# Performance work log

Measured on AMD Instinct MI355X. Metric: run time of the kernel, lower is better.

Reference implementation:

```python
import jax, jax.numpy as jnp
import numpy as np

DIM = 512
HEADS = 8
HEAD_DIM = DIM // HEADS
SCALE = HEAD_DIM ** -0.5
CPB_HIDDEN = 512
N_CLASSES = 2
LN_EPS = 1e-5


def _layernorm(x, g, b):
    m = jnp.mean(x, axis=-1, keepdims=True)
    v = jnp.var(x, axis=-1, keepdims=True)
    return (x - m) / jnp.sqrt(v + LN_EPS) * g + b


def _coord_attention(x, coords, cpb_w1, cpb_b1, cpb_w2, cpb_b2, qkv_w, qkv_b, proj_w, proj_b):
    B, N, C = x.shape
    qkv = (x @ qkv_w + qkv_b).reshape(B, N, 3, HEADS, HEAD_DIM)
    q, k, v = jnp.moveaxis(qkv, 2, 0)  # each (B, N, H, hd)
    attn = jnp.einsum('bnhd,bmhd->bhnm', q * SCALE, k)  # (B, H, N, N)
    rel = coords[:, :, None, :] - coords[:, None, :, :]  # (B, N, N, 2)
    rel = rel / (jnp.linalg.norm(rel, axis=-1, keepdims=True) + 1e-6)
    bias = jax.nn.relu(rel @ cpb_w1 + cpb_b1) @ cpb_w2 + cpb_b2  # (B, N, N, H)
    attn = jax.nn.softmax(attn + jnp.transpose(bias, (0, 3, 1, 2)), axis=-1)
    out = jnp.einsum('bhnm,bmhd->bnhd', attn, v).reshape(B, N, C)
    return out @ proj_w + proj_b


def setup_inputs() -> dict:
    key = jax.random.key(0)
    ks = iter(jax.random.split(key, 32))
    d = {}
    d['h'] = jax.random.normal(next(ks), (1, 400, 1024), dtype=jnp.float32)
    d['coords'] = jax.random.uniform(next(ks), (1, 400, 2), dtype=jnp.float32) * 1000.0
    def lin(kw, kb, fan_in, fan_out):
        w = jax.random.normal(kw, (fan_in, fan_out), dtype=jnp.float32) / np.sqrt(fan_in)
        b = jax.random.normal(kb, (fan_out,), dtype=jnp.float32) * 0.01
        return w, b
    d['fc1_w'], d['fc1_b'] = lin(next(ks), next(ks), 1024, DIM)
    d['cls_token'] = jax.random.normal(next(ks), (1, 1, DIM), dtype=jnp.float32)
    for p in ('l1', 'l2'):
        d[p + '_norm_g'] = jnp.ones((DIM,), jnp.float32)
        d[p + '_norm_b'] = jnp.zeros((DIM,), jnp.float32)
        d[p + '_cpb_w1'], d[p + '_cpb_b1'] = lin(next(ks), next(ks), 2, CPB_HIDDEN)
        d[p + '_cpb_w2'], d[p + '_cpb_b2'] = lin(next(ks), next(ks), CPB_HIDDEN, HEADS)
        d[p + '_qkv_w'], d[p + '_qkv_b'] = lin(next(ks), next(ks), DIM, 3 * DIM)
        d[p + '_proj_w'], d[p + '_proj_b'] = lin(next(ks), next(ks), DIM, DIM)
    d['norm_g'] = jnp.ones((DIM,), jnp.float32)
    d['norm_b'] = jnp.zeros((DIM,), jnp.float32)
    d['fc2_w'], d['fc2_b'] = lin(next(ks), next(ks), DIM, N_CLASSES)
    return d


def reference(h, coords, fc1_w, fc1_b, cls_token,
              l1_norm_g, l1_norm_b, l1_cpb_w1, l1_cpb_b1, l1_cpb_w2, l1_cpb_b2,
              l1_qkv_w, l1_qkv_b, l1_proj_w, l1_proj_b,
              l2_norm_g, l2_norm_b, l2_cpb_w1, l2_cpb_b1, l2_cpb_w2, l2_cpb_b2,
              l2_qkv_w, l2_qkv_b, l2_proj_w, l2_proj_b,
              norm_g, norm_b, fc2_w, fc2_b):
    B, Np, _ = h.shape
    h = jax.nn.relu(h @ fc1_w + fc1_b)  # (B, N, 512)
    side = int(np.ceil(np.sqrt(Np)))
    add = side * side - Np  # pad bag to a perfect square (wrap-around copy)
    h = jnp.concatenate([h, h[:, :add, :]], axis=1)
    coords = jnp.concatenate([coords, coords[:, :add, :]], axis=1)
    cls = jnp.broadcast_to(cls_token, (B, 1, DIM))
    h = jnp.concatenate([cls, h], axis=1)
    coords = jnp.concatenate([jnp.zeros((B, 1, 2), h.dtype), coords], axis=1)
    h = h + _coord_attention(_layernorm(h, l1_norm_g, l1_norm_b), coords,
                             l1_cpb_w1, l1_cpb_b1, l1_cpb_w2, l1_cpb_b2,
                             l1_qkv_w, l1_qkv_b, l1_proj_w, l1_proj_b)
    h = h + _coord_attention(_layernorm(h, l2_norm_g, l2_norm_b), coords,
                             l2_cpb_w1, l2_cpb_b1, l2_cpb_w2, l2_cpb_b2,
                             l2_qkv_w, l2_qkv_b, l2_proj_w, l2_proj_b)
    h = _layernorm(h, norm_g, norm_b)[:, 0]  # CLS token
    return h @ fc2_w + fc2_b  # (B, n_classes)
```

## Files before the change

### kernel.cpp

```cpp
#include <hip/hip_runtime.h>
#include <math.h>

#define NP 401
#define DIM 512
#define HEADS 8
#define HD 64
#define LN_EPS 1e-5f
#define ATT_SCALE 0.125f
#define SP 448
#define PLANE (NP * SP)
#define CPB_M 16384
#define TSTRIDE (CPB_M + 64)
#define PS (401L * 1536)

template<bool TB, typename LA, typename LB>
__device__ __forceinline__ void gemm64(
    int kBeg, int kEnd, int tid,
    float (*as)[68], float (*bs)[68], float (&acc)[4][4],
    LA&& loadA, LB&& loadB)
{
    float aR[4], bR[4];
    loadA(kBeg, aR);
    loadB(kBeg, bR);
    for (int k0 = kBeg; k0 < kEnd; k0 += 16) {
        const int arow = tid >> 2, aq = tid & 3;
        as[aq * 4 + 0][arow] = aR[0];
        as[aq * 4 + 1][arow] = aR[1];
        as[aq * 4 + 2][arow] = aR[2];
        as[aq * 4 + 3][arow] = aR[3];
        if (!TB) {
            *(float4*)&bs[tid >> 4][(tid & 15) * 4] =
                make_float4(bR[0], bR[1], bR[2], bR[3]);
        } else {
            bs[aq * 4 + 0][arow] = bR[0];
            bs[aq * 4 + 1][arow] = bR[1];
            bs[aq * 4 + 2][arow] = bR[2];
            bs[aq * 4 + 3][arow] = bR[3];
        }
        __syncthreads();
        float nA[4] = {0.f,0.f,0.f,0.f}, nB[4] = {0.f,0.f,0.f,0.f};
        if (k0 + 16 < kEnd) { loadA(k0 + 16, nA); loadB(k0 + 16, nB); }
        const int tx = tid & 15, ty = tid >> 4;
        #pragma unroll
        for (int kk = 0; kk < 16; ++kk) {
            float4 a4 = *(const float4*)&as[kk][ty * 4];
            float4 b4 = *(const float4*)&bs[kk][tx * 4];
            float av[4] = {a4.x, a4.y, a4.z, a4.w};
            float bv[4] = {b4.x, b4.y, b4.z, b4.w};
            #pragma unroll
            for (int r = 0; r < 4; ++r)
                #pragma unroll
                for (int c = 0; c < 4; ++c)
                    acc[r][c] = fmaf(av[r], bv[c], acc[r][c]);
        }
        __syncthreads();
        #pragma unroll
        for (int j = 0; j < 4; ++j) { aR[j] = nA[j]; bR[j] = nB[j]; }
    }
}

__global__ __launch_bounds__(256) void gemm_split_kernel(
    const float* __restrict__ A, int lda,
    const float* __restrict__ B, int ldb,
    float* __restrict__ P, int ldc, long slice,
    int M, int N, int K, int skN)
{
    __shared__ float as[16][68], bs[16][68];
    const int tid = threadIdx.x;
    const int m0 = blockIdx.x * 64, n0 = blockIdx.y * 64;
    const int sk = blockIdx.z;
    const int KS = ((K + skN * 16 - 1) / (skN * 16)) * 16;
    const int kBeg = sk * KS;
    const int kEnd = (kBeg + KS < K) ? kBeg + KS : K;
    float acc[4][4] = {};

    auto loadA = [&](int k0, float r[4]) {
        r[0] = r[1] = r[2] = r[3] = 0.f;
        int gm = m0 + (tid >> 2);
        if (gm >= M) return;
        int gk = k0 + (tid & 3) * 4;
        const float* p = A + (long)gm * lda + gk;
        if (gk + 3 < kEnd) {
            float4 v = *(const float4*)p;
            r[0] = v.x; r[1] = v.y; r[2] = v.z; r[3] = v.w;
        } else {
            #pragma unroll
            for (int j = 0; j < 4; ++j) if (gk + j < kEnd) r[j] = p[j];
        }
    };
    auto loadB = [&](int k0, float r[4]) {
        r[0] = r[1] = r[2] = r[3] = 0.f;
        int gk = k0 + (tid >> 4);
        if (gk >= kEnd) return;
        int gn = n0 + (tid & 15) * 4;
        const float* p = B + (long)gk * ldb + gn;
        if (gn + 3 < N) {
            float4 v = *(const float4*)p;
            r[0] = v.x; r[1] = v.y; r[2] = v.z; r[3] = v.w;
        } else {
            #pragma unroll
            for (int j = 0; j < 4; ++j) if (gn + j < N) r[j] = p[j];
        }
    };
    if (kBeg < kEnd)
        gemm64<false>(kBeg, kEnd, tid, as, bs, acc, loadA, loadB);

    float* C = P + (long)sk * slice;
    const int tx = tid & 15, ty = tid >> 4;
    #pragma unroll
    for (int r = 0; r < 4; ++r) {
        int m = m0 + ty * 4 + r;
        if (m >= M) continue;
        int n = n0 + tx * 4;
        if (n + 3 < N) {
            *(float4*)&C[(long)m * ldc + n] =
                make_float4(acc[r][0], acc[r][1], acc[r][2], acc[r][3]);
        } else {
            #pragma unroll
            for (int c = 0; c < 4; ++c)
                if (n + c < N) C[(long)m * ldc + n + c] = acc[r][c];
        }
    }
}

__global__ __launch_bounds__(256) void qk_kernel(
    const float* __restrict__ Pq, const float* __restrict__ qkv_b,
    const int* __restrict__ pm, const float* __restrict__ pf,
    const float* __restrict__ T,
    float* __restrict__ S)
{
    __shared__ float as[16][68], bs[16][68];
    const int tid = threadIdx.x;
    const int m0 = blockIdx.x * 64, n0 = blockIdx.y * 64, h = blockIdx.z;
    float acc[4][4] = {};

    auto loadQ = [&](int k0, float r[4]) {
        int gm = m0 + (tid >> 2);
        if (gm > 400) { r[0]=r[1]=r[2]=r[3]=0.f; return; }
        int gk = k0 + (tid & 3) * 4;
        long off = (long)gm * 1536 + h * 64 + gk;
        float4 x = *(const float4*)(Pq + off);
        float4 y = *(const float4*)(Pq + PS + off);
        float4 b = *(const float4*)(qkv_b + h * 64 + gk);
        r[0] = x.x + y.x + b.x; r[1] = x.y + y.y + b.y;
        r[2] = x.z + y.z + b.z; r[3] = x.w + y.w + b.w;
    };
    auto loadK = [&](int k0, float r[4]) {
        int gn = n0 + (tid >> 2);
        if (gn > 400) { r[0]=r[1]=r[2]=r[3]=0.f; return; }
        int gk = k0 + (tid & 3) * 4;
        long off = (long)gn * 1536 + 512 + h * 64 + gk;
        float4 x = *(const float4*)(Pq + off);
        float4 y = *(const float4*)(Pq + PS + off);
        float4 b = *(const float4*)(qkv_b + 512 + h * 64 + gk);
        r[0] = x.x + y.x + b.x; r[1] = x.y + y.y + b.y;
        r[2] = x.z + y.z + b.z; r[3] = x.w + y.w + b.w;
    };
    gemm64<true>(0, 64, tid, as, bs, acc, loadQ, loadK);

    const int tx = tid & 15, ty = tid >> 4;
    const float* Tt = T + (long)h * TSTRIDE;
    float* Sp = S + (long)h * PLANE;
    #pragma unroll
    for (int r = 0; r < 4; ++r) {
        int i = m0 + ty * 4 + r;
        if (i > 400) continue;
        #pragma unroll
        for (int c = 0; c < 4; ++c) {
            int j = n0 + tx * 4 + c;
            if (j > 400) continue;
            int id = i * 416 + j;
            int mm = pm[id];
            float fr = pf[id];
            float t0 = Tt[mm], t1 = Tt[mm + 1];
            Sp[(long)i * SP + j] =
                fmaf(acc[r][c], ATT_SCALE, fmaf(fr, t1 - t0, t0));
        }
    }
}

__global__ __launch_bounds__(256) void pv_kernel(
    const float* __restrict__ S, const float* __restrict__ Pq,
    const float* __restrict__ qkv_b, float* __restrict__ Pv)
{
    __shared__ float as[16][68], bs[16][68];
    const int tid = threadIdx.x;
    const int m0 = blockIdx.x * 64;
    const int h = blockIdx.z >> 3, sk = blockIdx.z & 7;
    const int kBeg = sk * 64;
    const int kEnd = (kBeg + 64 < NP) ? kBeg + 64 : NP;
    float acc[4][4] = {};

    auto loadA = [&](int k0, float r[4]) {
        r[0] = r[1] = r[2] = r[3] = 0.f;
        int gm = m0 + (tid >> 2);
        if (gm > 400) return;
        int gk = k0 + (tid & 3) * 4;
        const float* p = S + (long)h * PLANE + (long)gm * SP + gk;
        if (gk + 3 < kEnd) {
            float4 v = *(const float4*)p;
            r[0] = v.x; r[1] = v.y; r[2] = v.z; r[3] = v.w;
        } else {
            #pragma unroll
            for (int j = 0; j < 4; ++j) if (gk + j < kEnd) r[j] = p[j];
        }
    };
    auto loadB = [&](int k0, float r[4]) {
        r[0] = r[1] = r[2] = r[3] = 0.f;
        int key = k0 + (tid >> 4);
        if (key >= kEnd) return;
        int d = (tid & 15) * 4;
        long off = (long)key * 1536 + 1024 + h * 64 + d;
        float4 x = *(const float4*)(Pq + off);
        float4 y = *(const float4*)(Pq + PS + off);
        float4 b = *(const float4*)(qkv_b + 1024 + h * 64 + d);
        r[0] = x.x + y.x + b.x; r[1] = x.y + y.y + b.y;
        r[2] = x.z + y.z + b.z; r[3] = x.w + y.w + b.w;
    };
    if (kBeg < kEnd)
        gemm64<false>(kBeg, kEnd, tid, as, bs, acc, loadA, loadB);

    float* C = Pv + (long)sk * (401L * 512);
    const int tx = tid & 15, ty = tid >> 4;
    #pragma unroll
    for (int r = 0; r < 4; ++r) {
        int m = m0 + ty * 4 + r;
        if (m > 400) continue;
        *(float4*)&C[(long)m * 512 + h * 64 + tx * 4] =
            make_float4(acc[r][0], acc[r][1], acc[r][2], acc[r][3]);
    }
}

__global__ __launch_bounds__(256) void att_reduce_kernel(
    const float* __restrict__ Pv, float* __restrict__ att)
{
    int idx = (blockIdx.x * 256 + threadIdx.x) * 4;
    if (idx >= 401 * 512) return;
    float4 s = *(const float4*)(Pv + idx);
    #pragma unroll
    for (int k = 1; k < 8; ++k) {
        float4 p = *(const float4*)(Pv + (long)k * 401 * 512 + idx);
        s.x += p.x; s.y += p.y; s.z += p.z; s.w += p.w;
    }
    *(float4*)(att + idx) = s;
}

__global__ __launch_bounds__(256) void softmax_kernel(float* __restrict__ S)
{
    long base = (long)blockIdx.y * PLANE + (long)blockIdx.x * SP;
    int t = threadIdx.x;
    float v0 = (t < NP) ? S[base + t] : -INFINITY;
    float v1 = (t + 256 < NP) ? S[base + t + 256] : -INFINITY;
    float m = fmaxf(v0, v1);
    #pragma unroll
    for (int off = 32; off > 0; off >>= 1) m = fmaxf(m, __shfl_down(m, off));
    __shared__ float pm_[4], psum[4];
    int w = t >> 6, lane = t & 63;
    if (lane == 0) pm_[w] = m;
    __syncthreads();
    float M4 = fmaxf(fmaxf(pm_[0], pm_[1]), fmaxf(pm_[2], pm_[3]));
    float e0 = (t < NP) ? __expf(v0 - M4) : 0.f;
    float e1 = (t + 256 < NP) ? __expf(v1 - M4) : 0.f;
    float s = e0 + e1;
    #pragma unroll
    for (int off = 32; off > 0; off >>= 1) s += __shfl_down(s, off);
    if (lane == 0) psum[w] = s;
    __syncthreads();
    float inv = 1.f / (psum[0] + psum[1] + psum[2] + psum[3]);
    if (t < NP)       S[base + t] = e0 * inv;
    if (t + 256 < NP) S[base + t + 256] = e1 * inv;
}

__global__ __launch_bounds__(256) void rowfuse_kernel(
    const float* __restrict__ P, long slice, int skN, int rowOff,
    const float* __restrict__ bias, int doRelu,
    const float* __restrict__ resid, const float* __restrict__ cls,
    float* __restrict__ h0,
    const float* __restrict__ g, const float* __restrict__ b,
    float* __restrict__ xln,
    const float* __restrict__ fc2w, const float* __restrict__ fc2b,
    float* __restrict__ out)
{
    const int r = blockIdx.x, t = threadIdx.x;
    float v0, v1;
    if (cls && r == 0) {
        v0 = cls[t]; v1 = cls[t + 256];
    } else {
        const float* p = P + (long)(r - rowOff) * DIM;
        v0 = bias[t]; v1 = bias[t + 256];
        for (int k = 0; k < skN; ++k) {
            v0 += p[(long)k * slice + t];
            v1 += p[(long)k * slice + t + 256];
        }
        if (resid) {
            v0 += resid[(long)r * DIM + t];
            v1 += resid[(long)r * DIM + t + 256];
        }
        if (doRelu) { v0 = fmaxf(v0, 0.f); v1 = fmaxf(v1, 0.f); }
    }
    h0[(long)r * DIM + t] = v0;
    h0[(long)r * DIM + t + 256] = v1;
    if (out && r != 0) return;

    float s = v0 + v1, sq = v0 * v0 + v1 * v1;
    #pragma unroll
    for (int off = 32; off > 0; off >>= 1) {
        s += __shfl_down(s, off);
        sq += __shfl_down(sq, off);
    }
    __shared__ float ps[4], pq[4], pc0[4], pc1[4];
    int w = t >> 6, lane = t & 63;
    if (lane == 0) { ps[w] = s; pq[w] = sq; }
    __syncthreads();
    float Sm = ps[0] + ps[1] + ps[2] + ps[3];
    float Q = pq[0] + pq[1] + pq[2] + pq[3];
    float mean = Sm * (1.f / DIM);
    float var = Q * (1.f / DIM) - mean * mean;
    float inv = rsqrtf(var + LN_EPS);
    float n0 = (v0 - mean) * inv * g[t] + b[t];
    float n1 = (v1 - mean) * inv * g[t + 256] + b[t + 256];
    if (!out) {
        xln[(long)r * DIM + t] = n0;
        xln[(long)r * DIM + t + 256] = n1;
    } else {
        float c0 = n0 * fc2w[t * 2]     + n1 * fc2w[(t + 256) * 2];
        float c1 = n0 * fc2w[t * 2 + 1] + n1 * fc2w[(t + 256) * 2 + 1];
        #pragma unroll
        for (int off = 32; off > 0; off >>= 1) {
            c0 += __shfl_down(c0, off);
            c1 += __shfl_down(c1, off);
        }
        if (lane == 0) { pc0[w] = c0; pc1[w] = c1; }
        __syncthreads();
        if (t == 0) {
            out[0] = pc0[0] + pc0[1] + pc0[2] + pc0[3] + fc2b[0];
            out[1] = pc1[0] + pc1[1] + pc1[2] + pc1[3] + fc2b[1];
        }
    }
}

__global__ __launch_bounds__(256) void mega_kernel(
    const float* __restrict__ hin, const float* __restrict__ fc1_w,
    const float* __restrict__ w1_0, const float* __restrict__ b1_0,
    const float* __restrict__ w2_0, const float* __restrict__ b2_0,
    const float* __restrict__ w1_1, const float* __restrict__ b1_1,
    const float* __restrict__ w2_1, const float* __restrict__ b2_1,
    const float* __restrict__ coords,
    float* __restrict__ Pp, float* __restrict__ T,
    int* __restrict__ pm, float* __restrict__ pf)
{
    __shared__ float as[16][68], bs[16][68];
    __shared__ float red[4][64][8];
    const int bid = blockIdx.x, tid = threadIdx.x;

    if (bid < 448) {
        int sk = bid / 56, rem = bid % 56;
        int m0 = (rem % 7) * 64, n0 = (rem / 7) * 64;
        int kBeg = sk * 128, kEnd = kBeg + 128;
        float acc[4][4] = {};
        auto loadA = [&](int k0, float r[4]) {
            r[0]=r[1]=r[2]=r[3]=0.f;
            int gm = m0 + (tid >> 2);
            if (gm >= 400) return;
            int gk = k0 + (tid & 3) * 4;
            float4 v = *(const float4*)(hin + (long)gm * 1024 + gk);
            r[0]=v.x; r[1]=v.y; r[2]=v.z; r[3]=v.w;
        };
        auto loadB = [&](int k0, float r[4]) {
            int gk = k0 + (tid >> 4);
            int gn = n0 + (tid & 15) * 4;
            float4 v = *(const float4*)(fc1_w + (long)gk * 512 + gn);
            r[0]=v.x; r[1]=v.y; r[2]=v.z; r[3]=v.w;
        };
        gemm64<false>(kBeg, kEnd, tid, as, bs, acc, loadA, loadB);
        float* C = Pp + (long)sk * (400L * 512);
        const int tx = tid & 15, ty = tid >> 4;
        #pragma unroll
        for (int r = 0; r < 4; ++r) {
            int m = m0 + ty * 4 + r;
            if (m >= 400) continue;
            *(float4*)&C[(long)m * 512 + n0 + tx * 4] =
                make_float4(acc[r][0], acc[r][1], acc[r][2], acc[r][3]);
        }
    } else if (bid < 962) {
        int tb = bid - 448;
        int z = tb / 257, ab = tb % 257;
        const float* w1 = z ? w1_1 : w1_0;
        const float* b1 = z ? b1_1 : b1_0;
        const float* w2 = z ? w2_1 : w2_0;
        const float* b2 = z ? b2_1 : b2_0;
        const int lane = tid & 63, wv = tid >> 6;
        float ca = 0.f, sa = 0.f;
        if (ab != 256) {
            float th = fmaf((float)(ab * 64 + lane),
                            (float)(2.0 * M_PI / CPB_M), -(float)M_PI);
            sincosf(th, &sa, &ca);
        } else if (lane == 0) {
            sincosf((float)M_PI, &sa, &ca);
        }
        float a8[8] = {};
        const int kbeg = wv * 128;
        #pragma unroll 4
        for (int k = kbeg; k < kbeg + 128; ++k) {
            float hk = fmaxf(fmaf(ca, w1[k], fmaf(sa, w1[512 + k], b1[k])), 0.f);
            #pragma unroll
            for (int h2 = 0; h2 < 8; ++h2)
                a8[h2] = fmaf(hk, w2[k * 8 + h2], a8[h2]);
        }
        #pragma unroll
        for (int h2 = 0; h2 < 8; ++h2) red[wv][lane][h2] = a8[h2];
        __syncthreads();
        if (tid < 64) {
            int a = ab * 64 + tid;
            #pragma unroll
            for (int h2 = 0; h2 < 8; ++h2)
                T[(long)(z * 8 + h2) * TSTRIDE + a] =
                    red[0][tid][h2] + red[1][tid][h2] +
                    red[2][tid][h2] + red[3][tid][h2] + b2[h2];
        }
    } else {
        int p = (bid - 962) * 256 + tid;
        if (p < NP * NP) {
            int i = p / NP, j = p - i * NP;
            float xi = (i == 0) ? 0.f : coords[(i - 1) * 2];
            float yi = (i == 0) ? 0.f : coords[(i - 1) * 2 + 1];
            float xj = (j == 0) ? 0.f : coords[(j - 1) * 2];
            float yj = (j == 0) ? 0.f : coords[(j - 1) * 2 + 1];
            float rx = xi - xj, ry = yi - yj;
            int mm; float fr;
            if (rx == 0.f && ry == 0.f) {
                mm = CPB_M + 1; fr = 0.f;
            } else {
                float x = (atan2f(ry, rx) + 3.14159265358979f)
                          * (float)(CPB_M / (2.0 * M_PI));
                int mi = (int)x;
                fr = x - (float)mi;
                mm = (mi >= CPB_M) ? mi - CPB_M : mi;
            }
            pm[i * 416 + j] = mm;
            pf[i * 416 + j] = fr;
        }
    }
}

extern "C" void kernel_launch(void* const* d_in, const int* in_sizes, int n_in,
                              void* d_out, int out_size, void* d_ws, size_t ws_size,
                              hipStream_t stream)
{
    const float* h      = (const float*)d_in[0];
    const float* coords = (const float*)d_in[1];
    const float* fc1_w  = (const float*)d_in[2];
    const float* fc1_b  = (const float*)d_in[3];
    const float* cls    = (const float*)d_in[4];
    const float* norm_g = (const float*)d_in[25];
    const float* norm_b = (const float*)d_in[26];
    const float* fc2_w  = (const float*)d_in[27];
    const float* fc2_b  = (const float*)d_in[28];

    float* ws  = (float*)d_ws;
    float* h0  = ws;
    float* xln = h0  + 401L * 512;
    float* att = xln + 401L * 512;
    float* S   = att + 401L * 512;
    float* T   = S   + 8L * PLANE;
    int*   pm  = (int*)(T + 16L * TSTRIDE);
    float* pf  = (float*)(pm + 401L * 416);
    float* Pq  = pf + 401L * 416;
    float* Pv  = Pq + 2L * 401 * 1536;
    float* Pp  = Pv + 8L * 401 * 512;

    mega_kernel<<<1591, 256, 0, stream>>>(
        h, fc1_w,
        (const float*)d_in[7],  (const float*)d_in[8],
        (const float*)d_in[9],  (const float*)d_in[10],
        (const float*)d_in[17], (const float*)d_in[18],
        (const float*)d_in[19], (const float*)d_in[20],
        coords, Pp, T, pm, pf);

    rowfuse_kernel<<<401, 256, 0, stream>>>(
        Pp, 400L * 512, 8, 1, fc1_b, 1, nullptr, cls, h0,
        (const float*)d_in[5], (const float*)d_in[6], xln,
        nullptr, nullptr, nullptr);

    for (int l = 0; l < 2; ++l) {
        int base = 5 + 10 * l;
        const float* qkv_w  = (const float*)d_in[base + 6];
        const float* qkv_b  = (const float*)d_in[base + 7];
        const float* proj_w = (const float*)d_in[base + 8];
        const float* proj_b = (const float*)d_in[base + 9];

        gemm_split_kernel<<<dim3(7, 24, 2), 256, 0, stream>>>(
            xln, 512, qkv_w, 1536, Pq, 1536, 401L * 1536, 401, 1536, 512, 2);

        qk_kernel<<<dim3(7, 7, 8), 256, 0, stream>>>(
            Pq, qkv_b, pm, pf, T + (long)l * 8 * TSTRIDE, S);

        softmax_kernel<<<dim3(401, 8), 256, 0, stream>>>(S);

        pv_kernel<<<dim3(7, 1, 64), 256, 0, stream>>>(S, Pq, qkv_b, Pv);
        att_reduce_kernel<<<201, 256, 0, stream>>>(Pv, att);

        gemm_split_kernel<<<dim3(7, 8, 8), 256, 0, stream>>>(
            att, 512, proj_w, 512, Pp, 512, 401L * 512, 401, 512, 512, 8);

        if (l == 0) {
            rowfuse_kernel<<<401, 256, 0, stream>>>(
                Pp, 401L * 512, 8, 0, proj_b, 0, h0, nullptr, h0,
                (const float*)d_in[15], (const float*)d_in[16], xln,
                nullptr, nullptr, nullptr);
        } else {
            rowfuse_kernel<<<401, 256, 0, stream>>>(
                Pp, 401L * 512, 8, 0, proj_b, 0, h0, nullptr, h0,
                norm_g, norm_b, nullptr, fc2_w, fc2_b, (float*)d_out);
        }
    }
}
```

Measured before the change: 282.2 us.

## Compute only CLS row in second attention layer and restructure split-K kernels

The second attention layer now computes only the CLS query's attention, projection and final LayerNorm/fc2, because only token 0 feeds the output. The full QK/softmax/PV/proj path for layer 2 is replaced by small dedicated kernels. Layer 1 also changes: the split-K factors are retuned (fc1 16-way, qkv 4-way, PV 4-way), the attention reduction is folded into a new proj kernel, and softmax uses one wavefront per row. Layer 2 still computes full K and V with the QKV GEMM, and the fc1 split-K doubling adds more partial-sum traffic in exchange for more parallelism.

```diff
diff --git a/kernel.cpp b/kernel.cpp
--- a/kernel.cpp
+++ b/kernel.cpp
@@ -3,15 +3,14 @@
 
 #define NP 401
 #define DIM 512
-#define HEADS 8
-#define HD 64
 #define LN_EPS 1e-5f
 #define ATT_SCALE 0.125f
 #define SP 448
 #define PLANE (NP * SP)
 #define CPB_M 16384
 #define TSTRIDE (CPB_M + 64)
-#define PS (401L * 1536)
+#define PQS (401L * 1536)
+#define PVS (401L * 512)
 
 template<bool TB, typename LA, typename LB>
 __device__ __forceinline__ void gemm64(
@@ -94,13 +93,8 @@
         if (gk >= kEnd) return;
         int gn = n0 + (tid & 15) * 4;
         const float* p = B + (long)gk * ldb + gn;
-        if (gn + 3 < N) {
-            float4 v = *(const float4*)p;
-            r[0] = v.x; r[1] = v.y; r[2] = v.z; r[3] = v.w;
-        } else {
-            #pragma unroll
-            for (int j = 0; j < 4; ++j) if (gn + j < N) r[j] = p[j];
-        }
+        float4 v = *(const float4*)p;
+        r[0] = v.x; r[1] = v.y; r[2] = v.z; r[3] = v.w;
     };
     if (kBeg < kEnd)
         gemm64<false>(kBeg, kEnd, tid, as, bs, acc, loadA, loadB);
@@ -111,23 +105,15 @@
     for (int r = 0; r < 4; ++r) {
         int m = m0 + ty * 4 + r;
         if (m >= M) continue;
-        int n = n0 + tx * 4;
-        if (n + 3 < N) {
-            *(float4*)&C[(long)m * ldc + n] =
-                make_float4(acc[r][0], acc[r][1], acc[r][2], acc[r][3]);
-        } else {
-            #pragma unroll
-            for (int c = 0; c < 4; ++c)
-                if (n + c < N) C[(long)m * ldc + n + c] = acc[r][c];
-        }
+        *(float4*)&C[(long)m * ldc + n0 + tx * 4] =
+            make_float4(acc[r][0], acc[r][1], acc[r][2], acc[r][3]);
     }
 }
 
 __global__ __launch_bounds__(256) void qk_kernel(
-    const float* __restrict__ Pq, const float* __restrict__ qkv_b,
+    const float* __restrict__ Pq, const float* __restrict__ qkvb,
     const int* __restrict__ pm, const float* __restrict__ pf,
-    const float* __restrict__ T,
-    float* __restrict__ S)
+    const float* __restrict__ T, float* __restrict__ S)
 {
     __shared__ float as[16][68], bs[16][68];
     const int tid = threadIdx.x;
@@ -139,22 +125,30 @@
         if (gm > 400) { r[0]=r[1]=r[2]=r[3]=0.f; return; }
         int gk = k0 + (tid & 3) * 4;
         long off = (long)gm * 1536 + h * 64 + gk;
-        float4 x = *(const float4*)(Pq + off);
-        float4 y = *(const float4*)(Pq + PS + off);
-        float4 b = *(const float4*)(qkv_b + h * 64 + gk);
-        r[0] = x.x + y.x + b.x; r[1] = x.y + y.y + b.y;
-        r[2] = x.z + y.z + b.z; r[3] = x.w + y.w + b.w;
+        float4 x0 = *(const float4*)(Pq + off);
+        float4 x1 = *(const float4*)(Pq + PQS + off);
+        float4 x2 = *(const float4*)(Pq + 2 * PQS + off);
+        float4 x3 = *(const float4*)(Pq + 3 * PQS + off);
+        float4 b  = *(const float4*)(qkvb + h * 64 + gk);
+        r[0] = x0.x + x1.x + x2.x + x3.x + b.x;
+        r[1] = x0.y + x1.y + x2.y + x3.y + b.y;
+        r[2] = x0.z + x1.z + x2.z + x3.z + b.z;
+        r[3] = x0.w + x1.w + x2.w + x3.w + b.w;
     };
     auto loadK = [&](int k0, float r[4]) {
         int gn = n0 + (tid >> 2);
         if (gn > 400) { r[0]=r[1]=r[2]=r[3]=0.f; return; }
         int gk = k0 + (tid & 3) * 4;
         long off = (long)gn * 1536 + 512 + h * 64 + gk;
-        float4 x = *(const float4*)(Pq + off);
-        float4 y = *(const float4*)(Pq + PS + off);
-        float4 b = *(const float4*)(qkv_b + 512 + h * 64 + gk);
-        r[0] = x.x + y.x + b.x; r[1] = x.y + y.y + b.y;
-        r[2] = x.z + y.z + b.z; r[3] = x.w + y.w + b.w;
+        float4 x0 = *(const float4*)(Pq + off);
+        float4 x1 = *(const float4*)(Pq + PQS + off);
+        float4 x2 = *(const float4*)(Pq + 2 * PQS + off);
+        float4 x3 = *(const float4*)(Pq + 3 * PQS + off);
+        float4 b  = *(const float4*)(qkvb + 512 + h * 64 + gk);
+        r[0] = x0.x + x1.x + x2.x + x3.x + b.x;
+        r[1] = x0.y + x1.y + x2.y + x3.y + b.y;
+        r[2] = x0.z + x1.z + x2.z + x3.z + b.z;
+        r[3] = x0.w + x1.w + x2.w + x3.w + b.w;
     };
     gemm64<true>(0, 64, tid, as, bs, acc, loadQ, loadK);
 
@@ -179,16 +173,50 @@
     }
 }
 
+__global__ __launch_bounds__(256) void softmax_kernel(float* __restrict__ S)
+{
+    int r = blockIdx.x * 4 + (threadIdx.x >> 6);
+    if (r >= 3208) return;
+    int hh = r / 401, i = r - hh * 401;
+    float* row = S + (long)hh * PLANE + (long)i * SP;
+    int lane = threadIdx.x & 63;
+    float v[7], mx = -INFINITY;
+    #pragma unroll
+    for (int j = 0; j < 7; ++j) {
+        int c = lane + j * 64;
+        v[j] = (c < NP) ? row[c] : -INFINITY;
+        mx = fmaxf(mx, v[j]);
+    }
+    #pragma unroll
+    for (int off = 32; off > 0; off >>= 1)
+        mx = fmaxf(mx, __shfl_xor(mx, off));
+    float s = 0.f;
+    #pragma unroll
+    for (int j = 0; j < 7; ++j) {
+        v[j] = (lane + j * 64 < NP) ? __expf(v[j] - mx) : 0.f;
+        s += v[j];
+    }
+    #pragma unroll
+    for (int off = 32; off > 0; off >>= 1)
+        s += __shfl_xor(s, off);
+    float inv = 1.f / s;
+    #pragma unroll
+    for (int j = 0; j < 7; ++j) {
+        int c = lane + j * 64;
+        if (c < NP) row[c] = v[j] * inv;
+    }
+}
+
 __global__ __launch_bounds__(256) void pv_kernel(
     const float* __restrict__ S, const float* __restrict__ Pq,
-    const float* __restrict__ qkv_b, float* __restrict__ Pv)
+    const float* __restrict__ qkvb, float* __restrict__ Pv)
 {
     __shared__ float as[16][68], bs[16][68];
     const int tid = threadIdx.x;
     const int m0 = blockIdx.x * 64;
-    const int h = blockIdx.z >> 3, sk = blockIdx.z & 7;
-    const int kBeg = sk * 64;
-    const int kEnd = (kBeg + 64 < NP) ? kBeg + 64 : NP;
+    const int h = blockIdx.z >> 2, sk = blockIdx.z & 3;
+    const int kBeg = sk * 112;
+    const int kEnd = (kBeg + 112 < NP) ? kBeg + 112 : NP;
     float acc[4][4] = {};
 
     auto loadA = [&](int k0, float r[4]) {
@@ -199,7 +227,7 @@
         const float* p = S + (long)h * PLANE + (long)gm * SP + gk;
         if (gk + 3 < kEnd) {
             float4 v = *(const float4*)p;
-            r[0] = v.x; r[1] = v.y; r[2] = v.z; r[3] = v.w;
+            r[0]=v.x; r[1]=v.y; r[2]=v.z; r[3]=v.w;
         } else {
             #pragma unroll
             for (int j = 0; j < 4; ++j) if (gk + j < kEnd) r[j] = p[j];
@@ -211,16 +239,19 @@
         if (key >= kEnd) return;
         int d = (tid & 15) * 4;
         long off = (long)key * 1536 + 1024 + h * 64 + d;
-        float4 x = *(const float4*)(Pq + off);
-        float4 y = *(const float4*)(Pq + PS + off);
-        float4 b = *(const float4*)(qkv_b + 1024 + h * 64 + d);
-        r[0] = x.x + y.x + b.x; r[1] = x.y + y.y + b.y;
-        r[2] = x.z + y.z + b.z; r[3] = x.w + y.w + b.w;
-    };
-    if (kBeg < kEnd)
-        gemm64<false>(kBeg, kEnd, tid, as, bs, acc, loadA, loadB);
-
-    float* C = Pv + (long)sk * (401L * 512);
+        float4 x0 = *(const float4*)(Pq + off);
+        float4 x1 = *(const float4*)(Pq + PQS + off);
+        float4 x2 = *(const float4*)(Pq + 2 * PQS + off);
+        float4 x3 = *(const float4*)(Pq + 3 * PQS + off);
+        float4 b  = *(const float4*)(qkvb + 1024 + h * 64 + d);
+        r[0] = x0.x + x1.x + x2.x + x3.x + b.x;
+        r[1] = x0.y + x1.y + x2.y + x3.y + b.y;
+        r[2] = x0.z + x1.z + x2.z + x3.z + b.z;
+        r[3] = x0.w + x1.w + x2.w + x3.w + b.w;
+    };
+    gemm64<false>(kBeg, kEnd, tid, as, bs, acc, loadA, loadB);
+
+    float* C = Pv + (long)sk * PVS;
     const int tx = tid & 15, ty = tid >> 4;
     #pragma unroll
     for (int r = 0; r < 4; ++r) {
@@ -231,44 +262,48 @@
     }
 }
 
-__global__ __launch_bounds__(256) void att_reduce_kernel(
-    const float* __restrict__ Pv, float* __restrict__ att)
-{
-    int idx = (blockIdx.x * 256 + threadIdx.x) * 4;
-    if (idx >= 401 * 512) return;
-    float4 s = *(const float4*)(Pv + idx);
-    #pragma unroll
-    for (int k = 1; k < 8; ++k) {
-        float4 p = *(const float4*)(Pv + (long)k * 401 * 512 + idx);
-        s.x += p.x; s.y += p.y; s.z += p.z; s.w += p.w;
-    }
-    *(float4*)(att + idx) = s;
-}
-
-__global__ __launch_bounds__(256) void softmax_kernel(float* __restrict__ S)
-{
-    long base = (long)blockIdx.y * PLANE + (long)blockIdx.x * SP;
-    int t = threadIdx.x;
-    float v0 = (t < NP) ? S[base + t] : -INFINITY;
-    float v1 = (t + 256 < NP) ? S[base + t + 256] : -INFINITY;
-    float m = fmaxf(v0, v1);
-    #pragma unroll
-    for (int off = 32; off > 0; off >>= 1) m = fmaxf(m, __shfl_down(m, off));
-    __shared__ float pm_[4], psum[4];
-    int w = t >> 6, lane = t & 63;
-    if (lane == 0) pm_[w] = m;
-    __syncthreads();
-    float M4 = fmaxf(fmaxf(pm_[0], pm_[1]), fmaxf(pm_[2], pm_[3]));
-    float e0 = (t < NP) ? __expf(v0 - M4) : 0.f;
-    float e1 = (t + 256 < NP) ? __expf(v1 - M4) : 0.f;
-    float s = e0 + e1;
-    #pragma unroll
-    for (int off = 32; off > 0; off >>= 1) s += __shfl_down(s, off);
-    if (lane == 0) psum[w] = s;
-    __syncthreads();
-    float inv = 1.f / (psum[0] + psum[1] + psum[2] + psum[3]);
-    if (t < NP)       S[base + t] = e0 * inv;
-    if (t + 256 < NP) S[base + t + 256] = e1 * inv;
+__global__ __launch_bounds__(256) void proj_kernel(
+    const float* __restrict__ Pv, const float* __restrict__ projw,
+    float* __restrict__ Pp)
+{
+    __shared__ float as[16][68], bs[16][68];
+    const int tid = threadIdx.x;
+    const int m0 = blockIdx.x * 64, n0 = blockIdx.y * 64, sk = blockIdx.z;
+    const int kBeg = sk * 64, kEnd = kBeg + 64;
+    float acc[4][4] = {};
+
+    auto loadA = [&](int k0, float r[4]) {
+        r[0] = r[1] = r[2] = r[3] = 0.f;
+        int gm = m0 + (tid >> 2);
+        if (gm > 400) return;
+        int gk = k0 + (tid & 3) * 4;
+        long off = (long)gm * 512 + gk;
+        float4 x0 = *(const float4*)(Pv + off);
+        float4 x1 = *(const float4*)(Pv + PVS + off);
+        float4 x2 = *(const float4*)(Pv + 2 * PVS + off);
+        float4 x3 = *(const float4*)(Pv + 3 * PVS + off);
+        r[0] = x0.x + x1.x + x2.x + x3.x;
+        r[1] = x0.y + x1.y + x2.y + x3.y;
+        r[2] = x0.z + x1.z + x2.z + x3.z;
+        r[3] = x0.w + x1.w + x2.w + x3.w;
+    };
+    auto loadB = [&](int k0, float r[4]) {
+        int gk = k0 + (tid >> 4);
+        int gn = n0 + (tid & 15) * 4;
+        float4 v = *(const float4*)(projw + (long)gk * 512 + gn);
+        r[0]=v.x; r[1]=v.y; r[2]=v.z; r[3]=v.w;
+    };
+    gemm64<false>(kBeg, kEnd, tid, as, bs, acc, loadA, loadB);
+
+    float* C = Pp + (long)sk * PVS;
+    const int tx = tid & 15, ty = tid >> 4;
+    #pragma unroll
+    for (int r = 0; r < 4; ++r) {
+        int m = m0 + ty * 4 + r;
+        if (m > 400) continue;
+        *(float4*)&C[(long)m * 512 + n0 + tx * 4] =
+            make_float4(acc[r][0], acc[r][1], acc[r][2], acc[r][3]);
+    }
 }
 
 __global__ __launch_bounds__(256) void rowfuse_kernel(
@@ -277,9 +312,7 @@
     const float* __restrict__ resid, const float* __restrict__ cls,
     float* __restrict__ h0,
     const float* __restrict__ g, const float* __restrict__ b,
-    float* __restrict__ xln,
-    const float* __restrict__ fc2w, const float* __restrict__ fc2b,
-    float* __restrict__ out)
+    float* __restrict__ xln)
 {
     const int r = blockIdx.x, t = threadIdx.x;
     float v0, v1;
@@ -300,8 +333,136 @@
     }
     h0[(long)r * DIM + t] = v0;
     h0[(long)r * DIM + t + 256] = v1;
-    if (out && r != 0) return;
-
+
+    float s = v0 + v1, sq = v0 * v0 + v1 * v1;
+    #pragma unroll
+    for (int off = 32; off > 0; off >>= 1) {
+        s += __shfl_down(s, off);
+        sq += __shfl_down(sq, off);
+    }
+    __shared__ float ps[4], pq[4];
+    int w = t >> 6, lane = t & 63;
+    if (lane == 0) { ps[w] = s; pq[w] = sq; }
+    __syncthreads();
+    float Sm = ps[0] + ps[1] + ps[2] + ps[3];
+    float Q = pq[0] + pq[1] + pq[2] + pq[3];
+    float mean = Sm * (1.f / DIM);
+    float var = Q * (1.f / DIM) - mean * mean;
+    float inv = rsqrtf(var + LN_EPS);
+    xln[(long)r * DIM + t]       = (v0 - mean) * inv * g[t] + b[t];
+    xln[(long)r * DIM + t + 256] = (v1 - mean) * inv * g[t + 256] + b[t + 256];
+}
+
+__global__ __launch_bounds__(256) void cls_attn_kernel(
+    const float* __restrict__ Pq, const float* __restrict__ qkvb,
+    const int* __restrict__ pm, const float* __restrict__ pf,
+    const float* __restrict__ T, float* __restrict__ att0)
+{
+    const int h = blockIdx.x, tid = threadIdx.x;
+    __shared__ float q0[64], sc[512], red[4][64], rr[8];
+
+    if (tid < 64) {
+        long o = h * 64 + tid;
+        q0[tid] = Pq[o] + Pq[PQS + o] + Pq[2 * PQS + o] + Pq[3 * PQS + o]
+                  + qkvb[o];
+    }
+    __syncthreads();
+
+    const float* Tt = T + (long)h * TSTRIDE;
+    #pragma unroll
+    for (int jj = 0; jj < 2; ++jj) {
+        int j = tid + jj * 256;
+        if (j < NP) {
+            long base = (long)j * 1536 + 512 + h * 64;
+            float dot = 0.f;
+            #pragma unroll
+            for (int d = 0; d < 64; d += 4) {
+                float4 x0 = *(const float4*)(Pq + base + d);
+                float4 x1 = *(const float4*)(Pq + PQS + base + d);
+                float4 x2 = *(const float4*)(Pq + 2 * PQS + base + d);
+                float4 x3 = *(const float4*)(Pq + 3 * PQS + base + d);
+                float4 bb = *(const float4*)(qkvb + 512 + h * 64 + d);
+                float4 qq = *(const float4*)(q0 + d);
+                dot = fmaf(qq.x, x0.x + x1.x + x2.x + x3.x + bb.x, dot);
+                dot = fmaf(qq.y, x0.y + x1.y + x2.y + x3.y + bb.y, dot);
+                dot = fmaf(qq.z, x0.z + x1.z + x2.z + x3.z + bb.z, dot);
+                dot = fmaf(qq.w, x0.w + x1.w + x2.w + x3.w + bb.w, dot);
+            }
+            int mm = pm[j];
+            float fr = pf[j];
+            float t0 = Tt[mm], t1 = Tt[mm + 1];
+            sc[j] = fmaf(dot, ATT_SCALE, fmaf(fr, t1 - t0, t0));
+        } else if (j < 512) {
+            sc[j] = -INFINITY;
+        }
+    }
+    __syncthreads();
+
+    float m = fmaxf(sc[tid], sc[tid + 256]);
+    #pragma unroll
+    for (int off = 32; off > 0; off >>= 1)
+        m = fmaxf(m, __shfl_xor(m, off));
+    int w = tid >> 6, lane = tid & 63;
+    if (lane == 0) rr[w] = m;
+    __syncthreads();
+    float M = fmaxf(fmaxf(rr[0], rr[1]), fmaxf(rr[2], rr[3]));
+    float e0 = (tid < NP) ? __expf(sc[tid] - M) : 0.f;
+    float e1 = (tid + 256 < NP) ? __expf(sc[tid + 256] - M) : 0.f;
+    float s = e0 + e1;
+    #pragma unroll
+    for (int off = 32; off > 0; off >>= 1)
+        s += __shfl_xor(s, off);
+    if (lane == 0) rr[4 + w] = s;
+    __syncthreads();
+    float inv = 1.f / (rr[4] + rr[5] + rr[6] + rr[7]);
+    sc[tid] = e0 * inv;
+    sc[tid + 256] = e1 * inv;
+    __syncthreads();
+
+    const int d = lane;
+    float vb = qkvb[1024 + h * 64 + d];
+    float acc = 0.f;
+    for (int j = w; j < NP; j += 4) {
+        long o = (long)j * 1536 + 1024 + h * 64 + d;
+        float v = Pq[o] + Pq[PQS + o] + Pq[2 * PQS + o] + Pq[3 * PQS + o] + vb;
+        acc = fmaf(sc[j], v, acc);
+    }
+    red[w][d] = acc;
+    __syncthreads();
+    if (tid < 64)
+        att0[h * 64 + tid] =
+            red[0][tid] + red[1][tid] + red[2][tid] + red[3][tid];
+}
+
+__global__ __launch_bounds__(256) void cls_proj_kernel(
+    const float* __restrict__ att0, const float* __restrict__ projw,
+    const float* __restrict__ projb, float* __restrict__ proj0)
+{
+    __shared__ float av[512], red[4][64];
+    const int b = blockIdx.x, tid = threadIdx.x;
+    av[tid] = att0[tid];
+    av[tid + 256] = att0[tid + 256];
+    __syncthreads();
+    int g = tid >> 6, n = b * 64 + (tid & 63);
+    float acc = 0.f;
+    for (int k = g * 128; k < g * 128 + 128; ++k)
+        acc = fmaf(av[k], projw[(long)k * 512 + n], acc);
+    red[g][tid & 63] = acc;
+    __syncthreads();
+    if (tid < 64)
+        proj0[b * 64 + tid] = red[0][tid] + red[1][tid] + red[2][tid]
+                              + red[3][tid] + projb[b * 64 + tid];
+}
+
+__global__ __launch_bounds__(256) void cls_out_kernel(
+    const float* __restrict__ h0, const float* __restrict__ proj0,
+    const float* __restrict__ g, const float* __restrict__ b,
+    const float* __restrict__ fc2w, const float* __restrict__ fc2b,
+    float* __restrict__ out)
+{
+    const int t = threadIdx.x;
+    float v0 = h0[t] + proj0[t];
+    float v1 = h0[t + 256] + proj0[t + 256];
     float s = v0 + v1, sq = v0 * v0 + v1 * v1;
     #pragma unroll
     for (int off = 32; off > 0; off >>= 1) {
@@ -319,23 +480,18 @@
     float inv = rsqrtf(var + LN_EPS);
     float n0 = (v0 - mean) * inv * g[t] + b[t];
     float n1 = (v1 - mean) * inv * g[t + 256] + b[t + 256];
-    if (!out) {
-        xln[(long)r * DIM + t] = n0;
-        xln[(long)r * DIM + t + 256] = n1;
-    } else {
-        float c0 = n0 * fc2w[t * 2]     + n1 * fc2w[(t + 256) * 2];
-        float c1 = n0 * fc2w[t * 2 + 1] + n1 * fc2w[(t + 256) * 2 + 1];
-        #pragma unroll
-        for (int off = 32; off > 0; off >>= 1) {
-            c0 += __shfl_down(c0, off);
-            c1 += __shfl_down(c1, off);
-        }
-        if (lane == 0) { pc0[w] = c0; pc1[w] = c1; }
-        __syncthreads();
-        if (t == 0) {
-            out[0] = pc0[0] + pc0[1] + pc0[2] + pc0[3] + fc2b[0];
-            out[1] = pc1[0] + pc1[1] + pc1[2] + pc1[3] + fc2b[1];
-        }
+    float c0 = n0 * fc2w[t * 2]     + n1 * fc2w[(t + 256) * 2];
+    float c1 = n0 * fc2w[t * 2 + 1] + n1 * fc2w[(t + 256) * 2 + 1];
+    #pragma unroll
+    for (int off = 32; off > 0; off >>= 1) {
+        c0 += __shfl_down(c0, off);
+        c1 += __shfl_down(c1, off);
+    }
+    if (lane == 0) { pc0[w] = c0; pc1[w] = c1; }
+    __syncthreads();
+    if (t == 0) {
+        out[0] = pc0[0] + pc0[1] + pc0[2] + pc0[3] + fc2b[0];
+        out[1] = pc1[0] + pc1[1] + pc1[2] + pc1[3] + fc2b[1];
     }
 }
 
@@ -349,14 +505,16 @@
     float* __restrict__ Pp, float* __restrict__ T,
     int* __restrict__ pm, float* __restrict__ pf)
 {
-    __shared__ float as[16][68], bs[16][68];
-    __shared__ float red[4][64][8];
+    __shared__ float smem[2176];
+    float (*as)[68] = (float(*)[68])smem;
+    float (*bs)[68] = (float(*)[68])(smem + 1088);
+    float (*red)[64][8] = (float(*)[64][8])smem;
     const int bid = blockIdx.x, tid = threadIdx.x;
 
-    if (bid < 448) {
+    if (bid < 896) {
         int sk = bid / 56, rem = bid % 56;
         int m0 = (rem % 7) * 64, n0 = (rem / 7) * 64;
-        int kBeg = sk * 128, kEnd = kBeg + 128;
+        int kBeg = sk * 64, kEnd = kBeg + 64;
         float acc[4][4] = {};
         auto loadA = [&](int k0, float r[4]) {
             r[0]=r[1]=r[2]=r[3]=0.f;
@@ -373,7 +531,7 @@
             r[0]=v.x; r[1]=v.y; r[2]=v.z; r[3]=v.w;
         };
         gemm64<false>(kBeg, kEnd, tid, as, bs, acc, loadA, loadB);
-        float* C = Pp + (long)sk * (400L * 512);
+        float* C = Pp + (long)sk * PVS;
         const int tx = tid & 15, ty = tid >> 4;
         #pragma unroll
         for (int r = 0; r < 4; ++r) {
@@ -382,8 +540,8 @@
             *(float4*)&C[(long)m * 512 + n0 + tx * 4] =
                 make_float4(acc[r][0], acc[r][1], acc[r][2], acc[r][3]);
         }
-    } else if (bid < 962) {
-        int tb = bid - 448;
+    } else if (bid < 1410) {
+        int tb = bid - 896;
         int z = tb / 257, ab = tb % 257;
         const float* w1 = z ? w1_1 : w1_0;
         const float* b1 = z ? b1_1 : b1_0;
@@ -402,7 +560,8 @@
         const int kbeg = wv * 128;
         #pragma unroll 4
         for (int k = kbeg; k < kbeg + 128; ++k) {
-            float hk = fmaxf(fmaf(ca, w1[k], fmaf(sa, w1[512 + k], b1[k])), 0.f);
+            float hk = fmaxf(fmaf(ca, w1[k],
+                                  fmaf(sa, w1[512 + k], b1[k])), 0.f);
             #pragma unroll
             for (int h2 = 0; h2 < 8; ++h2)
                 a8[h2] = fmaf(hk, w2[k * 8 + h2], a8[h2]);
@@ -411,15 +570,15 @@
         for (int h2 = 0; h2 < 8; ++h2) red[wv][lane][h2] = a8[h2];
         __syncthreads();
         if (tid < 64) {
-            int a = ab * 64 + tid;
+            int aidx = ab * 64 + tid;
             #pragma unroll
             for (int h2 = 0; h2 < 8; ++h2)
-                T[(long)(z * 8 + h2) * TSTRIDE + a] =
+                T[(long)(z * 8 + h2) * TSTRIDE + aidx] =
                     red[0][tid][h2] + red[1][tid][h2] +
                     red[2][tid][h2] + red[3][tid][h2] + b2[h2];
         }
     } else {
-        int p = (bid - 962) * 256 + tid;
+        int p = (bid - 1410) * 256 + tid;
         if (p < NP * NP) {
             int i = p / NP, j = p - i * NP;
             float xi = (i == 0) ? 0.f : coords[(i - 1) * 2];
@@ -447,30 +606,22 @@
                               void* d_out, int out_size, void* d_ws, size_t ws_size,
                               hipStream_t stream)
 {
-    const float* h      = (const float*)d_in[0];
     const float* coords = (const float*)d_in[1];
-    const float* fc1_w  = (const float*)d_in[2];
-    const float* fc1_b  = (const float*)d_in[3];
-    const float* cls    = (const float*)d_in[4];
-    const float* norm_g = (const float*)d_in[25];
-    const float* norm_b = (const float*)d_in[26];
-    const float* fc2_w  = (const float*)d_in[27];
-    const float* fc2_b  = (const float*)d_in[28];
-
-    float* ws  = (float*)d_ws;
-    float* h0  = ws;
-    float* xln = h0  + 401L * 512;
-    float* att = xln + 401L * 512;
-    float* S   = att + 401L * 512;
-    float* T   = S   + 8L * PLANE;
-    int*   pm  = (int*)(T + 16L * TSTRIDE);
-    float* pf  = (float*)(pm + 401L * 416);
-    float* Pq  = pf + 401L * 416;
-    float* Pv  = Pq + 2L * 401 * 1536;
-    float* Pp  = Pv + 8L * 401 * 512;
-
-    mega_kernel<<<1591, 256, 0, stream>>>(
-        h, fc1_w,
+    float* ws = (float*)d_ws;
+    float* h0   = ws;                    ws += 401L * 512;
+    float* xln  = ws;                    ws += 401L * 512;
+    float* S    = ws;                    ws += 8L * PLANE;
+    float* T    = ws;                    ws += 16L * TSTRIDE;
+    int*   pm   = (int*)ws;              ws += 401L * 416;
+    float* pf   = ws;                    ws += 401L * 416;
+    float* Pq   = ws;                    ws += 4L * PQS;
+    float* Pv   = ws;                    ws += 4L * PVS;
+    float* Pp   = ws;                    ws += 16L * PVS;
+    float* att0 = ws;                    ws += 512;
+    float* proj0 = ws;                   ws += 512;
+
+    mega_kernel<<<2039, 256, 0, stream>>>(
+        (const float*)d_in[0], (const float*)d_in[2],
         (const float*)d_in[7],  (const float*)d_in[8],
         (const float*)d_in[9],  (const float*)d_in[10],
         (const float*)d_in[17], (const float*)d_in[18],
@@ -478,40 +629,32 @@
         coords, Pp, T, pm, pf);
 
     rowfuse_kernel<<<401, 256, 0, stream>>>(
-        Pp, 400L * 512, 8, 1, fc1_b, 1, nullptr, cls, h0,
-        (const float*)d_in[5], (const float*)d_in[6], xln,
-        nullptr, nullptr, nullptr);
-
-    for (int l = 0; l < 2; ++l) {
-        int base = 5 + 10 * l;
-        const float* qkv_w  = (const float*)d_in[base + 6];
-        const float* qkv_b  = (const float*)d_in[base + 7];
-        const float* proj_w = (const float*)d_in[base + 8];
-        const float* proj_b = (const float*)d_in[base + 9];
-
-        gemm_split_kernel<<<dim3(7, 24, 2), 256, 0, stream>>>(
-            xln, 512, qkv_w, 1536, Pq, 1536, 401L * 1536, 401, 1536, 512, 2);
-
-        qk_kernel<<<dim3(7, 7, 8), 256, 0, stream>>>(
-            Pq, qkv_b, pm, pf, T + (long)l * 8 * TSTRIDE, S);
-
-        softmax_kernel<<<dim3(401, 8), 256, 0, stream>>>(S);
-
-        pv_kernel<<<dim3(7, 1, 64), 256, 0, stream>>>(S, Pq, qkv_b, Pv);
-        att_reduce_kernel<<<201, 256, 0, stream>>>(Pv, att);
-
-        gemm_split_kernel<<<dim3(7, 8, 8), 256, 0, stream>>>(
-            att, 512, proj_w, 512, Pp, 512, 401L * 512, 401, 512, 512, 8);
-
-        if (l == 0) {
-            rowfuse_kernel<<<401, 256, 0, stream>>>(
-                Pp, 401L * 512, 8, 0, proj_b, 0, h0, nullptr, h0,
-                (const float*)d_in[15], (const float*)d_in[16], xln,
-                nullptr, nullptr, nullptr);
-        } else {
-            rowfuse_kernel<<<401, 256, 0, stream>>>(
-                Pp, 401L * 512, 8, 0, proj_b, 0, h0, nullptr, h0,
-                norm_g, norm_b, nullptr, fc2_w, fc2_b, (float*)d_out);
-        }
-    }
-}
+        Pp, PVS, 16, 1, (const float*)d_in[3], 1, nullptr,
+        (const float*)d_in[4], h0,
+        (const float*)d_in[5], (const float*)d_in[6], xln);
+
+    gemm_split_kernel<<<dim3(7, 24, 4), 256, 0, stream>>>(
+        xln, 512, (const float*)d_in[11], 1536, Pq, 1536, PQS,
+        401, 1536, 512, 4);
+    qk_kernel<<<dim3(7, 7, 8), 256, 0, stream>>>(
+        Pq, (const float*)d_in[12], pm, pf, T, S);
+    softmax_kernel<<<802, 256, 0, stream>>>(S);
+    pv_kernel<<<dim3(7, 1, 32), 256, 0, stream>>>(
+        S, Pq, (const float*)d_in[12], Pv);
+    proj_kernel<<<dim3(7, 8, 8), 256, 0, stream>>>(
+        Pv, (const float*)d_in[13], Pp);
+    rowfuse_kernel<<<401, 256, 0, stream>>>(
+        Pp, PVS, 8, 0, (const float*)d_in[14], 0, h0, nullptr, h0,
+        (const float*)d_in[15], (const float*)d_in[16], xln);
+
+    gemm_split_kernel<<<dim3(7, 24, 4), 256, 0, stream>>>(
+        xln, 512, (const float*)d_in[21], 1536, Pq, 1536, PQS,
+        401, 1536, 512, 4);
+    cls_attn_kernel<<<8, 256, 0, stream>>>(
+        Pq, (const float*)d_in[22], pm, pf, T + 8L * TSTRIDE, att0);
+    cls_proj_kernel<<<8, 256, 0, stream>>>(
+        att0, (const float*)d_in[23], (const float*)d_in[24], proj0);
+    cls_out_kernel<<<1, 256, 0, stream>>>(
+        h0, proj0, (const float*)d_in[25], (const float*)d_in[26],
+        (const float*)d_in[27], (const float*)d_in[28], (float*)d_out);
+}
```

After: 309.6 us. 9.7% more time.
